# Kernel tuning notes

Hardware: AMD Instinct MI355X
Metric: run time of the kernel (lower is better)

Reference implementation:

```python
import jax, jax.numpy as jnp
import numpy as np

N_HEAD, M_DIM, K_DIM, V_DIM = 16, 1024, 64, 64
LN_EPS = 1e-5


def setup_inputs() -> dict:
    key = jax.random.key(0)
    ks = jax.random.split(key, 10)
    B, L = 4, 2048
    q = jax.random.normal(ks[0], (B, L, M_DIM), dtype=jnp.float32)
    k = jax.random.normal(ks[1], (B, L, M_DIM), dtype=jnp.float32)
    v = jax.random.normal(ks[2], (B, L, M_DIM), dtype=jnp.float32)
    s = 1.0 / np.sqrt(M_DIM)
    W_qs = jax.random.normal(ks[3], (M_DIM, N_HEAD * K_DIM), dtype=jnp.float32) * s
    W_ks = jax.random.normal(ks[4], (M_DIM, N_HEAD * K_DIM), dtype=jnp.float32) * s
    W_vs = jax.random.normal(ks[5], (M_DIM, N_HEAD * V_DIM), dtype=jnp.float32) * s
    fc_w = jax.random.normal(ks[6], (N_HEAD * V_DIM, M_DIM), dtype=jnp.float32) * (1.0 / np.sqrt(N_HEAD * V_DIM))
    fc_b = jnp.zeros((M_DIM,), dtype=jnp.float32)
    ln_g = jnp.ones((M_DIM,), dtype=jnp.float32)
    ln_b = jnp.zeros((M_DIM,), dtype=jnp.float32)
    return {"q": q, "k": k, "v": v, "W_qs": W_qs, "W_ks": W_ks, "W_vs": W_vs,
            "fc_w": fc_w, "fc_b": fc_b, "ln_g": ln_g, "ln_b": ln_b}


def reference(q, k, v, W_qs, W_ks, W_vs, fc_w, fc_b, ln_g, ln_b):
    B, Lq, _ = q.shape
    residual = q
    # project and split heads: [B, L, H, D]
    qh = (q @ W_qs).reshape(B, Lq, N_HEAD, K_DIM)
    kh = (k @ W_ks).reshape(B, k.shape[1], N_HEAD, K_DIM)
    vh = (v @ W_vs).reshape(B, v.shape[1], N_HEAD, V_DIM)
    temperature = np.power(K_DIM, 0.5).astype(np.float32)
    # attention scores [B, H, Lq, Lk]
    attn = jnp.einsum('bqhd,bkhd->bhqk', qh, kh) / temperature
    attn = jax.nn.softmax(attn, axis=-1)
    out = jnp.einsum('bhqk,bkhd->bqhd', attn, vh).reshape(B, Lq, N_HEAD * V_DIM)
    out = out @ fc_w + fc_b
    x = out + residual
    mu = jnp.mean(x, axis=-1, keepdims=True)
    var = jnp.mean(jnp.square(x - mu), axis=-1, keepdims=True)
    return (x - mu) * jax.lax.rsqrt(var + LN_EPS) * ln_g + ln_b
```

## Files before the change

kernel.cpp:

```cpp
#include <hip/hip_runtime.h>
#include <math.h>

#define NHEAD 16
#define MDIM  1024
#define KD    64
#define BATCH 4
#define SEQ   2048
#define MROWS (BATCH*SEQ)

using short8 = __attribute__((ext_vector_type(8))) short;
using f4     = __attribute__((ext_vector_type(4))) float;
using f16x   = __attribute__((ext_vector_type(16))) float;

__device__ inline short f2bf(float x) {
  union { float f; unsigned u; } v; v.f = x;
  unsigned r = v.u + 0x7fffu + ((v.u >> 16) & 1u);
  return (short)(r >> 16);
}

__device__ __forceinline__ float fast_exp2(float x) {
#if __has_builtin(__builtin_amdgcn_exp2f)
  return __builtin_amdgcn_exp2f(x);
#else
  return exp2f(x);
#endif
}

__device__ __forceinline__ int pack_bf16(float lo, float hi) {
#if __has_builtin(__builtin_amdgcn_cvt_pk_bf16_f32)
  auto t = __builtin_amdgcn_cvt_pk_bf16_f32(lo, hi);
  int r; __builtin_memcpy(&r, &t, 4); return r;
#else
  unsigned u0 = __float_as_uint(lo) + 0x8000u;
  unsigned u1 = __float_as_uint(hi) + 0x8000u;
  return (int)__builtin_amdgcn_perm(u1, u0, 0x07060302u);
#endif
}

__device__ __forceinline__ void g2l16(const void* g, void* l) {
  __builtin_amdgcn_global_load_lds((const __attribute__((address_space(1))) unsigned int*)g,
                                   (__attribute__((address_space(3))) unsigned int*)l, 16, 0, 0);
}

#define AHIP_WAIT_LGKM0 asm volatile("s_waitcnt lgkmcnt(0)" ::: "memory")
#define AHIP_WAIT_VM4   asm volatile("s_waitcnt vmcnt(4)" ::: "memory")
#define AHIP_WAIT_VM0   asm volatile("s_waitcnt vmcnt(0)" ::: "memory")
#define AHIP_SFENCE     __builtin_amdgcn_sched_barrier(0)
#define AHIP_BAR        __builtin_amdgcn_s_barrier()

__global__ void wtrans_kernel(const float* __restrict__ w0, const float* __restrict__ w1,
                              const float* __restrict__ w2, const float* __restrict__ w3,
                              short* __restrict__ o0, short* __restrict__ o1,
                              short* __restrict__ o2, short* __restrict__ o3) {
  int z = blockIdx.z;
  const float* in = z == 0 ? w0 : (z == 1 ? w1 : (z == 2 ? w2 : w3));
  short* out = z == 0 ? o0 : (z == 1 ? o1 : (z == 2 ? o2 : o3));
  __shared__ float t[32][33];
  int bx = blockIdx.x * 32, by = blockIdx.y * 32;
  int tx = threadIdx.x, ty = threadIdx.y;
#pragma unroll
  for (int i = 0; i < 4; i++)
    t[ty + i * 8][tx] = in[(size_t)(by + ty + i * 8) * MDIM + bx + tx];
  __syncthreads();
#pragma unroll
  for (int i = 0; i < 4; i++)
    out[(size_t)(bx + ty + i * 8) * MDIM + by + tx] = f2bf(t[tx][ty + i * 8]);
}

__global__ void cvt_kernel(const float* __restrict__ q, const float* __restrict__ k,
                           const float* __restrict__ v, short* __restrict__ qb,
                           short* __restrict__ kb, short* __restrict__ vb) {
  const float* in = blockIdx.y == 0 ? q : (blockIdx.y == 1 ? k : v);
  short* out = blockIdx.y == 0 ? qb : (blockIdx.y == 1 ? kb : vb);
  size_t i = (size_t)blockIdx.x * 256 + threadIdx.x;
  float4 a = ((const float4*)in)[2 * i];
  float4 b = ((const float4*)in)[2 * i + 1];
  short8 s = {f2bf(a.x), f2bf(a.y), f2bf(a.z), f2bf(a.w),
              f2bf(b.x), f2bf(b.y), f2bf(b.z), f2bf(b.w)};
  ((short8*)out)[i] = s;
}

#define G8_PROLOGUE(Ab, Bt)                                                            \
  int tid = threadIdx.x, wid = tid >> 6, lane = tid & 63;                              \
  int quad = lane >> 4, low = lane & 15;                                               \
  int l8 = lane & 7, lr = lane >> 3;                                                   \
  int wrow = (wid >> 2) * 64, wcol = (wid & 3) * 32;                                   \
  const short* aS = Ab + (size_t)(m0 + wid * 16 + lr) * 1024 + (l8 ^ lr) * 8;          \
  const short* bS = Bt + (size_t)(n0 + wid * 16 + lr) * 1024 + (l8 ^ lr) * 8;          \
  auto stage = [&](int t, int b) {                                                     \
    const short* a = aS + t * 64;                                                      \
    const short* bb = bS + t * 64;                                                     \
    short* ad = &As[b][wid * 1024];                                                    \
    short* bd = &Bs[b][wid * 1024];                                                    \
    g2l16(a, ad);                                                                      \
    g2l16(a + 8 * 1024, ad + 512);                                                     \
    g2l16(bb, bd);                                                                     \
    g2l16(bb + 8 * 1024, bd + 512);                                                    \
  };                                                                                   \
  f4 acc[4][2];                                                                        \
  _Pragma("unroll")                                                                    \
  for (int mf = 0; mf < 4; mf++)                                                       \
    _Pragma("unroll")                                                                  \
    for (int nf = 0; nf < 2; nf++) {                                                   \
      acc[mf][nf][0] = 0.f; acc[mf][nf][1] = 0.f;                                      \
      acc[mf][nf][2] = 0.f; acc[mf][nf][3] = 0.f;                                      \
    }                                                                                  \
  stage(0, 0);                                                                         \
  stage(1, 1);                                                                         \
  AHIP_WAIT_VM4; AHIP_SFENCE; AHIP_BAR; AHIP_SFENCE;

#define G8_MAIN_LOOP()                                                                 \
  for (int t = 0; t < 16; ++t) {                                                       \
    const int cur = t & 1;                                                             \
    short8 af[2][4], bfv[2][2];                                                        \
    _Pragma("unroll")                                                                  \
    for (int kk = 0; kk < 2; kk++) {                                                   \
      _Pragma("unroll")                                                                \
      for (int mf = 0; mf < 4; mf++)                                                   \
        af[kk][mf] = *(const short8*)&As[cur][(wrow + mf * 16 + low) * 64 +            \
                                              (((kk * 4 + quad) ^ (low & 7)) * 8)];    \
      _Pragma("unroll")                                                                \
      for (int nf = 0; nf < 2; nf++)                                                   \
        bfv[kk][nf] = *(const short8*)&Bs[cur][(wcol + nf * 16 + low) * 64 +           \
                                               (((kk * 4 + quad) ^ (low & 7)) * 8)];   \
    }                                                                                  \
    AHIP_WAIT_LGKM0; AHIP_SFENCE;                                                      \
    AHIP_BAR; AHIP_SFENCE;                                                             \
    if (t + 2 < 16) stage(t + 2, cur);                                                 \
    __builtin_amdgcn_s_setprio(1);                                                     \
    _Pragma("unroll")                                                                  \
    for (int kk = 0; kk < 2; kk++)                                                     \
      _Pragma("unroll")                                                                \
      for (int mf = 0; mf < 4; mf++)                                                   \
        _Pragma("unroll")                                                              \
        for (int nf = 0; nf < 2; nf++)                                                 \
          acc[mf][nf] = __builtin_amdgcn_mfma_f32_16x16x32_bf16(af[kk][mf],            \
                          bfv[kk][nf], acc[mf][nf], 0, 0, 0);                          \
    __builtin_amdgcn_s_setprio(0);                                                     \
    AHIP_SFENCE;                                                                       \
    if (t + 2 < 16) { AHIP_WAIT_VM4; } else { AHIP_WAIT_VM0; }                         \
    AHIP_SFENCE; AHIP_BAR; AHIP_SFENCE;                                                \
  }

__launch_bounds__(512, 4)
__global__ void gemm_qkv_kernel(const short* __restrict__ qb, const short* __restrict__ kb,
                                const short* __restrict__ vb, const short* __restrict__ Wqt,
                                const short* __restrict__ Wkt, const short* __restrict__ Wvt,
                                short* __restrict__ Qh, short* __restrict__ Kh,
                                short* __restrict__ Vt) {
  __shared__ __attribute__((aligned(16))) short As[2][128 * 64];
  __shared__ __attribute__((aligned(16))) short Bs[2][128 * 64];
  int z = blockIdx.z;
  const short* Ab = z == 0 ? qb : (z == 1 ? kb : vb);
  const short* Bt = z == 0 ? Wqt : (z == 1 ? Wkt : Wvt);
  int m0 = blockIdx.x * 128, n0 = blockIdx.y * 128;

  G8_PROLOGUE(Ab, Bt)
  G8_MAIN_LOOP()

  float scale = z == 0 ? 0.18033688011112042f : 1.0f;
  short* dst = z == 0 ? Qh : (z == 1 ? Kh : Vt);
#pragma unroll
  for (int mf = 0; mf < 4; mf++)
#pragma unroll
    for (int nf = 0; nf < 2; nf++)
#pragma unroll
      for (int r2 = 0; r2 < 4; r2++) {
        int gr = m0 + wrow + mf * 16 + quad * 4 + r2;
        int gc = n0 + wcol + nf * 16 + low;
        float val = acc[mf][nf][r2];
        int b = gr >> 11, l = gr & 2047, h = gc >> 6, d = gc & 63;
        if (z < 2)
          dst[(((size_t)(b * NHEAD + h)) * SEQ + l) * KD + d] = f2bf(val * scale);
        else
          dst[(((size_t)(b * NHEAD + h)) * KD + d) * SEQ + l] = f2bf(val);
      }
}

__launch_bounds__(512, 4)
__global__ void gemm_fc_kernel(const short* __restrict__ Ab, const short* __restrict__ Bt,
                               float* __restrict__ dst, const float* __restrict__ bias,
                               const float* __restrict__ res) {
  __shared__ __attribute__((aligned(16))) short As[2][128 * 64];
  __shared__ __attribute__((aligned(16))) short Bs[2][128 * 64];
  int m0 = blockIdx.x * 128, n0 = blockIdx.y * 128;

  G8_PROLOGUE(Ab, Bt)
  G8_MAIN_LOOP()

#pragma unroll
  for (int mf = 0; mf < 4; mf++)
#pragma unroll
    for (int nf = 0; nf < 2; nf++)
#pragma unroll
      for (int r2 = 0; r2 < 4; r2++) {
        int gr = m0 + wrow + mf * 16 + quad * 4 + r2;
        int gc = n0 + wcol + nf * 16 + low;
        dst[(size_t)gr * 1024 + gc] = acc[mf][nf][r2] + bias[gc] + res[(size_t)gr * 1024 + gc];
      }
}

__launch_bounds__(512, 4)
__global__ void attn_kernel(const short* __restrict__ Qh, const short* __restrict__ Kh,
                            const short* __restrict__ Vt, short* __restrict__ Out) {
  __shared__ __attribute__((aligned(16))) short KT[2][64 * 64];
  __shared__ __attribute__((aligned(16))) short VT[2][64 * 64];
  int tid = threadIdx.x;
  int wave = tid >> 6, lane = tid & 63;
  int l = lane & 31, hi = lane >> 5;
  int bh = blockIdx.y;
  int q0 = blockIdx.x * 256 + wave * 32;

  const short* Qb = Qh + (size_t)bh * SEQ * KD;
  const short* Kb = Kh + (size_t)bh * SEQ * KD;
  const short* Vb = Vt + (size_t)bh * KD * SEQ;

  int srow = lane >> 3;
  int sch = (lane & 7) ^ srow;
  const short* kS = Kb + (size_t)(wave * 8 + srow) * KD + sch * 8;
  const short* vS = Vb + (size_t)(wave * 8 + srow) * SEQ + sch * 8;

  auto stage = [&](int k0, int b) {
    g2l16(kS + (size_t)k0 * KD, &KT[b][wave * 512]);
    g2l16(vS + k0, &VT[b][wave * 512]);
  };

  short8 qf[4];
#pragma unroll
  for (int ks = 0; ks < 4; ks++)
    qf[ks] = *(const short8*)&Qb[(size_t)(q0 + l) * KD + ks * 16 + hi * 8];

  f16x Oacc[2], lacc, fz;
#pragma unroll
  for (int i = 0; i < 16; i++) { Oacc[0][i] = 0.f; Oacc[1][i] = 0.f; lacc[i] = 0.f; fz[i] = 0.f; }
  const short8 onesb = {0x3F80, 0x3F80, 0x3F80, 0x3F80, 0x3F80, 0x3F80, 0x3F80, 0x3F80};

  stage(0, 0);
  __syncthreads();

  for (int c = 0; c < SEQ / 64; c++) {
    int b = c & 1;
    if (c + 1 < SEQ / 64) stage((c + 1) * 64, b ^ 1);

#pragma unroll
    for (int nt = 0; nt < 2; nt++) {
      short8 kf[4];
#pragma unroll
      for (int ks = 0; ks < 4; ks++)
        kf[ks] = *(const short8*)&KT[b][(nt * 32 + l) * 64 + (((ks * 2 + hi) ^ (l & 7)) * 8)];

      f16x S;
      __builtin_amdgcn_s_setprio(1);
      S = __builtin_amdgcn_mfma_f32_32x32x16_bf16(kf[0], qf[0], fz, 0, 0, 0);
      S = __builtin_amdgcn_mfma_f32_32x32x16_bf16(kf[1], qf[1], S, 0, 0, 0);
      S = __builtin_amdgcn_mfma_f32_32x32x16_bf16(kf[2], qf[2], S, 0, 0, 0);
      S = __builtin_amdgcn_mfma_f32_32x32x16_bf16(kf[3], qf[3], S, 0, 0, 0);
      __builtin_amdgcn_s_setprio(0);

      int u[8];
#pragma unroll
      for (int i = 0; i < 8; i++)
        u[i] = pack_bf16(fast_exp2(S[2 * i]), fast_exp2(S[2 * i + 1]));
      asm("v_permlane32_swap_b32 %0, %1" : "+v"(u[0]), "+v"(u[2]));
      asm("v_permlane32_swap_b32 %0, %1" : "+v"(u[1]), "+v"(u[3]));
      asm("v_permlane32_swap_b32 %0, %1" : "+v"(u[4]), "+v"(u[6]));
      asm("v_permlane32_swap_b32 %0, %1" : "+v"(u[5]), "+v"(u[7]));
      short8 pa0, pa1;
      {
        int t0[4] = {u[0], u[1], u[2], u[3]};
        int t1[4] = {u[4], u[5], u[6], u[7]};
        __builtin_memcpy(&pa0, t0, 16);
        __builtin_memcpy(&pa1, t1, 16);
      }

      __builtin_amdgcn_s_setprio(1);
      lacc = __builtin_amdgcn_mfma_f32_32x32x16_bf16(pa0, onesb, lacc, 0, 0, 0);
      lacc = __builtin_amdgcn_mfma_f32_32x32x16_bf16(pa1, onesb, lacc, 0, 0, 0);

#pragma unroll
      for (int dt = 0; dt < 2; dt++) {
        short8 vf0 = *(const short8*)&VT[b][(dt * 32 + l) * 64 + (((nt * 4 + 0 + hi) ^ (l & 7)) * 8)];
        short8 vf1 = *(const short8*)&VT[b][(dt * 32 + l) * 64 + (((nt * 4 + 2 + hi) ^ (l & 7)) * 8)];
        Oacc[dt] = __builtin_amdgcn_mfma_f32_32x32x16_bf16(pa0, vf0, Oacc[dt], 0, 0, 0);
        Oacc[dt] = __builtin_amdgcn_mfma_f32_32x32x16_bf16(pa1, vf1, Oacc[dt], 0, 0, 0);
      }
      __builtin_amdgcn_s_setprio(0);
    }
    __syncthreads();
  }

  int bb = bh >> 4, h = bh & 15;
#pragma unroll
  for (int r = 0; r < 16; r++) {
    int qrow = q0 + (r & 3) + 8 * (r >> 2) + 4 * hi;
    float iv = 1.0f / lacc[r];
#pragma unroll
    for (int dt = 0; dt < 2; dt++) {
      size_t idx = ((size_t)(bb * SEQ + qrow)) * 1024 + h * 64 + dt * 32 + l;
      Out[idx] = f2bf(Oacc[dt][r] * iv);
    }
  }
}

__launch_bounds__(256)
__global__ void ln_kernel(const float* __restrict__ x, const float* __restrict__ g,
                          const float* __restrict__ b, float* __restrict__ out) {
  int row = blockIdx.x, tid = threadIdx.x;
  const float4* xr = (const float4*)(x + (size_t)row * 1024);
  float4 v = xr[tid];
  float s = v.x + v.y + v.z + v.w;
  float q = v.x * v.x + v.y * v.y + v.z * v.z + v.w * v.w;
#pragma unroll
  for (int o = 32; o > 0; o >>= 1) { s += __shfl_xor(s, o); q += __shfl_xor(q, o); }
  __shared__ float ss[4], sq[4];
  if ((tid & 63) == 0) { ss[tid >> 6] = s; sq[tid >> 6] = q; }
  __syncthreads();
  if (tid == 0) {
    float S = ss[0] + ss[1] + ss[2] + ss[3];
    float Q = sq[0] + sq[1] + sq[2] + sq[3];
    float mean = S * (1.f / 1024.f);
    float var = Q * (1.f / 1024.f) - mean * mean;
    ss[0] = mean; sq[0] = rsqrtf(var + 1e-5f);
  }
  __syncthreads();
  float mean = ss[0], rs = sq[0];
  const float4* g4 = (const float4*)g;
  const float4* b4 = (const float4*)b;
  float4 gg = g4[tid], bb = b4[tid], o;
  o.x = (v.x - mean) * rs * gg.x + bb.x;
  o.y = (v.y - mean) * rs * gg.y + bb.y;
  o.z = (v.z - mean) * rs * gg.z + bb.z;
  o.w = (v.w - mean) * rs * gg.w + bb.w;
  ((float4*)(out + (size_t)row * 1024))[tid] = o;
}

extern "C" void kernel_launch(void* const* d_in, const int* in_sizes, int n_in,
                              void* d_out, int out_size, void* d_ws, size_t ws_size,
                              hipStream_t stream) {
  const float* q   = (const float*)d_in[0];
  const float* k   = (const float*)d_in[1];
  const float* v   = (const float*)d_in[2];
  const float* Wq  = (const float*)d_in[3];
  const float* Wk  = (const float*)d_in[4];
  const float* Wv  = (const float*)d_in[5];
  const float* fcw = (const float*)d_in[6];
  const float* fcb = (const float*)d_in[7];
  const float* lng = (const float*)d_in[8];
  const float* lnb = (const float*)d_in[9];
  float* out = (float*)d_out;

  char* ws = (char*)d_ws;
  const size_t MB = 1024 * 1024;
  short* Wqt = (short*)(ws + 0 * MB);
  short* Wkt = (short*)(ws + 2 * MB);
  short* Wvt = (short*)(ws + 4 * MB);
  short* fct = (short*)(ws + 6 * MB);
  short* qb  = (short*)(ws + 8 * MB);
  short* kb  = (short*)(ws + 24 * MB);
  short* vb  = (short*)(ws + 40 * MB);
  short* Kh  = (short*)(ws + 8 * MB);
  short* Vt  = (short*)(ws + 24 * MB);
  short* Ao  = (short*)(ws + 40 * MB);
  short* Qh  = (short*)(ws + 56 * MB);
  float* X   = (float*)(ws + 8 * MB);

  wtrans_kernel<<<dim3(32, 32, 4), dim3(32, 8), 0, stream>>>(Wq, Wk, Wv, fcw, Wqt, Wkt, Wvt, fct);

  cvt_kernel<<<dim3(MROWS * MDIM / 8 / 256, 3), 256, 0, stream>>>(q, k, v, qb, kb, vb);

  gemm_qkv_kernel<<<dim3(64, 8, 3), 512, 0, stream>>>(qb, kb, vb, Wqt, Wkt, Wvt, Qh, Kh, Vt);

  attn_kernel<<<dim3(SEQ / 256, BATCH * NHEAD), 512, 0, stream>>>(Qh, Kh, Vt, Ao);

  gemm_fc_kernel<<<dim3(64, 8), 512, 0, stream>>>(Ao, fct, X, fcb, q);

  ln_kernel<<<MROWS, 256, 0, stream>>>(X, lng, lnb, out);
}
```

Before: 347.3 us.

## Split attention KV range across two wave groups with LDS reduction

```diff
diff --git a/kernel.cpp b/kernel.cpp
--- a/kernel.cpp
+++ b/kernel.cpp
@@ -200,7 +200,7 @@
       }
 }
 
-__launch_bounds__(512, 4)
+__launch_bounds__(512, 8)
 __global__ void attn_kernel(const short* __restrict__ Qh, const short* __restrict__ Kh,
                             const short* __restrict__ Vt, short* __restrict__ Out) {
   __shared__ __attribute__((aligned(16))) short KT[2][64 * 64];
@@ -208,8 +208,12 @@
   int tid = threadIdx.x;
   int wave = tid >> 6, lane = tid & 63;
   int l = lane & 31, hi = lane >> 5;
-  int bh = blockIdx.y;
-  int q0 = blockIdx.x * 256 + wave * 32;
+  int grp = wave >> 2, wg = wave & 3;
+  int bx = blockIdx.x, by = blockIdx.y;
+  int bh = bx + (by & 7) * 8;
+  int qc = by >> 3;
+  int q0 = qc * 128 + wg * 32;
+  int kvbase = grp * 1024;
 
   const short* Qb = Qh + (size_t)bh * SEQ * KD;
   const short* Kb = Kh + (size_t)bh * SEQ * KD;
@@ -217,12 +221,16 @@
 
   int srow = lane >> 3;
   int sch = (lane & 7) ^ srow;
-  const short* kS = Kb + (size_t)(wave * 8 + srow) * KD + sch * 8;
-  const short* vS = Vb + (size_t)(wave * 8 + srow) * SEQ + sch * 8;
-
-  auto stage = [&](int k0, int b) {
-    g2l16(kS + (size_t)k0 * KD, &KT[b][wave * 512]);
-    g2l16(vS + k0, &VT[b][wave * 512]);
+  const short* kS0 = Kb + (size_t)(kvbase + wg * 16 + srow) * KD + sch * 8;
+  const short* kS1 = kS0 + (size_t)8 * KD;
+  const short* vS0 = Vb + (size_t)(wg * 16 + srow) * SEQ + kvbase + sch * 8;
+  const short* vS1 = vS0 + (size_t)8 * SEQ;
+
+  auto stage = [&](int k0) {
+    g2l16(kS0 + (size_t)k0 * KD, &KT[grp][wg * 1024]);
+    g2l16(kS1 + (size_t)k0 * KD, &KT[grp][wg * 1024 + 512]);
+    g2l16(vS0 + k0, &VT[grp][wg * 1024]);
+    g2l16(vS1 + k0, &VT[grp][wg * 1024 + 512]);
   };
 
   short8 qf[4];
@@ -230,28 +238,27 @@
   for (int ks = 0; ks < 4; ks++)
     qf[ks] = *(const short8*)&Qb[(size_t)(q0 + l) * KD + ks * 16 + hi * 8];
 
-  f16x Oacc[2], lacc, fz;
-#pragma unroll
-  for (int i = 0; i < 16; i++) { Oacc[0][i] = 0.f; Oacc[1][i] = 0.f; lacc[i] = 0.f; fz[i] = 0.f; }
+  f16x Oacc[2], lacc;
+#pragma unroll
+  for (int i = 0; i < 16; i++) { Oacc[0][i] = 0.f; Oacc[1][i] = 0.f; lacc[i] = 0.f; }
   const short8 onesb = {0x3F80, 0x3F80, 0x3F80, 0x3F80, 0x3F80, 0x3F80, 0x3F80, 0x3F80};
 
-  stage(0, 0);
-  __syncthreads();
-
-  for (int c = 0; c < SEQ / 64; c++) {
-    int b = c & 1;
-    if (c + 1 < SEQ / 64) stage((c + 1) * 64, b ^ 1);
-
+  stage(0);
+  __syncthreads();
+
+  for (int c = 0; c < 16; c++) {
 #pragma unroll
     for (int nt = 0; nt < 2; nt++) {
       short8 kf[4];
 #pragma unroll
       for (int ks = 0; ks < 4; ks++)
-        kf[ks] = *(const short8*)&KT[b][(nt * 32 + l) * 64 + (((ks * 2 + hi) ^ (l & 7)) * 8)];
+        kf[ks] = *(const short8*)&KT[grp][(nt * 32 + l) * 64 + (((ks * 2 + hi) ^ (l & 7)) * 8)];
 
       f16x S;
+#pragma unroll
+      for (int i = 0; i < 16; i++) S[i] = 0.f;
       __builtin_amdgcn_s_setprio(1);
-      S = __builtin_amdgcn_mfma_f32_32x32x16_bf16(kf[0], qf[0], fz, 0, 0, 0);
+      S = __builtin_amdgcn_mfma_f32_32x32x16_bf16(kf[0], qf[0], S, 0, 0, 0);
       S = __builtin_amdgcn_mfma_f32_32x32x16_bf16(kf[1], qf[1], S, 0, 0, 0);
       S = __builtin_amdgcn_mfma_f32_32x32x16_bf16(kf[2], qf[2], S, 0, 0, 0);
       S = __builtin_amdgcn_mfma_f32_32x32x16_bf16(kf[3], qf[3], S, 0, 0, 0);
@@ -279,25 +286,57 @@
 
 #pragma unroll
       for (int dt = 0; dt < 2; dt++) {
-        short8 vf0 = *(const short8*)&VT[b][(dt * 32 + l) * 64 + (((nt * 4 + 0 + hi) ^ (l & 7)) * 8)];
-        short8 vf1 = *(const short8*)&VT[b][(dt * 32 + l) * 64 + (((nt * 4 + 2 + hi) ^ (l & 7)) * 8)];
+        short8 vf0 = *(const short8*)&VT[grp][(dt * 32 + l) * 64 + (((nt * 4 + 0 + hi) ^ (l & 7)) * 8)];
+        short8 vf1 = *(const short8*)&VT[grp][(dt * 32 + l) * 64 + (((nt * 4 + 2 + hi) ^ (l & 7)) * 8)];
         Oacc[dt] = __builtin_amdgcn_mfma_f32_32x32x16_bf16(pa0, vf0, Oacc[dt], 0, 0, 0);
         Oacc[dt] = __builtin_amdgcn_mfma_f32_32x32x16_bf16(pa1, vf1, Oacc[dt], 0, 0, 0);
       }
       __builtin_amdgcn_s_setprio(0);
     }
     __syncthreads();
-  }
-
-  int bb = bh >> 4, h = bh & 15;
-#pragma unroll
-  for (int r = 0; r < 16; r++) {
-    int qrow = q0 + (r & 3) + 8 * (r >> 2) + 4 * hi;
-    float iv = 1.0f / lacc[r];
-#pragma unroll
-    for (int dt = 0; dt < 2; dt++) {
-      size_t idx = ((size_t)(bb * SEQ + qrow)) * 1024 + h * 64 + dt * 32 + l;
-      Out[idx] = f2bf(Oacc[dt][r] * iv);
+    if (c + 1 < 16) stage((c + 1) * 64);
+    __syncthreads();
+  }
+
+  float* kf32 = (float*)&KT[0][0];
+  float* vf32 = (float*)&VT[0][0];
+  if (grp == 1) {
+#pragma unroll
+    for (int i = 0; i < 16; i++) {
+      kf32[wg * 1024 + i * 64 + lane] = Oacc[0][i];
+      vf32[wg * 1024 + i * 64 + lane] = Oacc[1][i];
+    }
+  }
+  __syncthreads();
+  if (grp == 0) {
+#pragma unroll
+    for (int i = 0; i < 16; i++) {
+      Oacc[0][i] += kf32[wg * 1024 + i * 64 + lane];
+      Oacc[1][i] += vf32[wg * 1024 + i * 64 + lane];
+    }
+  }
+  __syncthreads();
+  if (grp == 1) {
+#pragma unroll
+    for (int i = 0; i < 16; i++)
+      kf32[wg * 1024 + i * 64 + lane] = lacc[i];
+  }
+  __syncthreads();
+  if (grp == 0) {
+#pragma unroll
+    for (int i = 0; i < 16; i++)
+      lacc[i] += kf32[wg * 1024 + i * 64 + lane];
+
+    int bb = bh >> 4, h = bh & 15;
+#pragma unroll
+    for (int r = 0; r < 16; r++) {
+      int qrow = q0 + (r & 3) + 8 * (r >> 2) + 4 * hi;
+      float iv = 1.0f / lacc[r];
+#pragma unroll
+      for (int dt = 0; dt < 2; dt++) {
+        size_t idx = ((size_t)(bb * SEQ + qrow)) * 1024 + h * 64 + dt * 32 + l;
+        Out[idx] = f2bf(Oacc[dt][r] * iv);
+      }
     }
   }
 }
@@ -370,7 +409,7 @@
 
   gemm_qkv_kernel<<<dim3(64, 8, 3), 512, 0, stream>>>(qb, kb, vb, Wqt, Wkt, Wvt, Qh, Kh, Vt);
 
-  attn_kernel<<<dim3(SEQ / 256, BATCH * NHEAD), 512, 0, stream>>>(Qh, Kh, Vt, Ao);
+  attn_kernel<<<dim3(8, 128), 512, 0, stream>>>(Qh, Kh, Vt, Ao);
 
   gemm_fc_kernel<<<dim3(64, 8), 512, 0, stream>>>(Ao, fct, X, fcb, q);
 
```

Result: slower. 1.348 ms (+288.2%).
